# Performance work log

Hardware: AMD Instinct MI355X
Metric: run time of the kernel (lower is better)

## Reference

```python
import jax, jax.numpy as jnp
import numpy as np

B, T, D = 32, 256, 512
P, V = 2048, 40000
DFF = 2148
K_CONCEPT = 50
K_PHENO = 10
EPS = 1e-6


def setup_inputs() -> dict:
    key = jax.random.key(0)
    ks = jax.random.split(key, 10)
    return {
        "visit_embeddings": jax.random.normal(ks[0], (B, T, D), jnp.float32) * 0.05,
        "visit_mask": jax.random.randint(ks[1], (B, T), 0, 2, jnp.int32),
        "embedding_matrix": jax.random.normal(ks[2], (V, D), jnp.float32) * 0.05,
        "phenotype_embeddings": jax.random.normal(ks[3], (P, D), jnp.float32) * 0.05,
        "w1": jax.random.normal(ks[4], (D, DFF), jnp.float32) * (1.0 / np.sqrt(D)),
        "b1": jnp.zeros((DFF,), jnp.float32),
        "w2": jax.random.normal(ks[5], (DFF, D), jnp.float32) * (1.0 / np.sqrt(DFF)),
        "b2": jnp.zeros((D,), jnp.float32),
        "ln1_g": jnp.ones((D,), jnp.float32),
        "ln1_b": jnp.zeros((D,), jnp.float32),
        "ln2_g": jnp.ones((D,), jnp.float32),
        "ln2_b": jnp.zeros((D,), jnp.float32),
    }


def _layer_norm(x, g, b):
    mu = jnp.mean(x, axis=-1, keepdims=True)
    var = jnp.mean(jnp.square(x - mu), axis=-1, keepdims=True)
    return (x - mu) * jax.lax.rsqrt(var + EPS) * g + b


def _smallest_k(x, k):
    # top_k of -x selects the k smallest values per row
    return -jax.lax.top_k(-x, k)[0]


def reference(visit_embeddings, visit_mask, embedding_matrix, phenotype_embeddings,
              w1, b1, w2, b2, ln1_g, ln1_b, ln2_g, ln2_b):
    # mask: original mask==1 means padded; converted mask is 1.0 for valid positions
    conv_mask = (1.0 - visit_mask.astype(jnp.float32))[:, :, None]  # [B,T,1]

    # phenotype attention: softmax over (logits * mask)  (faithful to TF code)
    logits = jnp.einsum('btd,pd->btp', visit_embeddings, phenotype_embeddings) * conv_mask
    probs = jax.nn.softmax(logits, axis=-1)  # [B,T,P]

    # phenotype-concept euclidean distance metric (cdist + row-wise smallest-k)
    r_p = jnp.sum(phenotype_embeddings * phenotype_embeddings, axis=1)[:, None]  # [P,1]
    r_c = jnp.sum(embedding_matrix * embedding_matrix, axis=1)[None, :]          # [1,V]
    d_pc = jnp.sqrt(r_p + r_c - 2.0 * phenotype_embeddings @ embedding_matrix.T)  # [P,V]
    phenotype_concept_dist = jnp.mean(_smallest_k(d_pc, K_CONCEPT))

    # phenotype probability entropy metric
    entropy = -jnp.sum(probs * jnp.log(probs) * conv_mask, axis=-1)  # [B,T]

    # phenotype-phenotype squared-distance metrics
    d_pp = r_p - 2.0 * phenotype_embeddings @ phenotype_embeddings.T + r_p.T  # [P,P]
    near = _smallest_k(d_pp, K_PHENO)  # [P,K_PHENO]
    phe_inv_loss = jnp.mean(jnp.exp(-near))
    phe_dist_metric = jnp.mean(near)
    phe_dist_var = jnp.var(near)

    # residual + FFN block (dropout is identity at inference)
    ctx = probs @ phenotype_embeddings  # [B,T,D]
    out1 = _layer_norm(visit_embeddings + ctx, ln1_g, ln1_b)
    ffn = jnp.maximum(out1 @ w1 + b1, 0.0) @ w2 + b2
    out2 = _layer_norm(out1 + ffn, ln2_g, ln2_b)

    return (out2, probs, phenotype_concept_dist, entropy,
            phe_inv_loss, phe_dist_metric, phe_dist_var)
```

## Files before the change

### kernel.cpp

```cpp
#include <hip/hip_runtime.h>
#include <stdint.h>
#include <stddef.h>

#define BATCH 32
#define TLEN 256
#define DIM 512
#define PHE 2048
#define VOC 40000
#define VOCP 40960
#define DFF 2148
#define DFFP2 2304
#define BT 8192
#define KC 50
#define KP 10
#define CHUNK 8192
#define NCHUNK 5
#define LNEPS 1e-6f
#define BIGF 1e30f

typedef unsigned short u16;
typedef __attribute__((ext_vector_type(8))) short short8;
typedef __attribute__((ext_vector_type(8))) unsigned short ushort8;
typedef __attribute__((ext_vector_type(4))) float floatx4;

__device__ inline u16 f2bf(float f) {
  union { float f; unsigned int u; } v; v.f = f;
  unsigned int u = v.u;
  return (u16)((u + 0x7fffu + ((u >> 16) & 1u)) >> 16);
}

__device__ inline unsigned int f2mono(float f) {
  union { float f; unsigned int u; } c; c.f = f;
  return (c.u & 0x80000000u) ? ~c.u : (c.u | 0x80000000u);
}
__device__ inline float mono2f(unsigned int u) {
  union { unsigned int u; float f; } c;
  c.u = (u & 0x80000000u) ? (u & 0x7FFFFFFFu) : ~u;
  return c.f;
}
__device__ inline unsigned int mono16(u16 u) {
  return (u & 0x8000u) ? (u16)~u : (u16)(u | 0x8000u);
}
__device__ inline float mono2f16(unsigned int k) {
  unsigned int ub = (k & 0x8000u) ? (k & 0x7FFFu) : ((~k) & 0xFFFFu);
  union { unsigned int u; float f; } c; c.u = ub << 16;
  return c.f;
}

__device__ inline void load_lds16(const void* g, void* l) {
  __builtin_amdgcn_global_load_lds(
      (const __attribute__((address_space(1))) unsigned int*)g,
      (__attribute__((address_space(3))) unsigned int*)l, 16, 0, 0);
}

__device__ inline float waveRedSum(float v) {
  #pragma unroll
  for (int off = 32; off > 0; off >>= 1) v += __shfl_down(v, off);
  return v;
}
__device__ inline float waveRedMax(float v) {
  #pragma unroll
  for (int off = 32; off > 0; off >>= 1) v = fmaxf(v, __shfl_down(v, off));
  return v;
}
__device__ inline float blockRedSum(float v) {
  __shared__ float sm[8];
  int lane = threadIdx.x & 63, w = threadIdx.x >> 6, nw = blockDim.x >> 6;
  v = waveRedSum(v);
  __syncthreads();
  if (lane == 0) sm[w] = v;
  __syncthreads();
  float r = 0.f;
  for (int i = 0; i < nw; ++i) r += sm[i];
  return r;
}
__device__ inline float blockRedMax(float v) {
  __shared__ float sm2[8];
  int lane = threadIdx.x & 63, w = threadIdx.x >> 6, nw = blockDim.x >> 6;
  v = waveRedMax(v);
  __syncthreads();
  if (lane == 0) sm2[w] = v;
  __syncthreads();
  float r = -BIGF;
  for (int i = 0; i < nw; ++i) r = fmaxf(r, sm2[i]);
  return r;
}
__device__ inline double blockRedSumD(double v) {
  __shared__ double red[256];
  int tid = threadIdx.x;
  __syncthreads();
  red[tid] = v;
  __syncthreads();
  for (int s = 128; s > 0; s >>= 1) {
    if (tid < s) red[tid] += red[tid + s];
    __syncthreads();
  }
  return red[0];
}

__device__ inline void hist_add2(int* hist, int digit, bool pred) {
  int lane = threadIdx.x & 63;
  unsigned long long act = __ballot(pred);
  if (!act) return;
  int src = __ffsll((long long)act) - 1;
  int ld = __shfl(digit, src);
  unsigned long long m = __ballot(pred && digit == ld);
  if (__popcll(m) >= 32) {
    if (lane == src) atomicAdd(&hist[ld], (int)__popcll(m));
    if ((act & ~m) & (1ull << lane)) atomicAdd(&hist[digit], 1);
  } else {
    if (pred) atomicAdd(&hist[digit], 1);
  }
}

__global__ void k_sentinel(float* out) { out[0] = -12345.0f; }

__global__ void k_cvt(const float* __restrict__ src, u16* __restrict__ dst, int n) {
  int i = blockIdx.x * blockDim.x + threadIdx.x;
  int stride = gridDim.x * blockDim.x;
  for (; i < n; i += stride) dst[i] = f2bf(src[i]);
}

__global__ void k_transpose(const float* __restrict__ src, int R, int C,
                            u16* __restrict__ dst, int DR, int DC) {
  int i = blockIdx.x * blockDim.x + threadIdx.x;
  if (i >= DR * DC) return;
  int r = i / DC, c = i % DC;
  float v = (r < C && c < R) ? src[(size_t)c * C + r] : 0.f;
  dst[i] = f2bf(v);
}

__global__ void k_rownorm(const float* __restrict__ src, float* __restrict__ out, int ncols) {
  int row = blockIdx.x;
  const float* p = src + (size_t)row * ncols;
  float s = 0.f;
  for (int i = threadIdx.x; i < ncols; i += blockDim.x) { float v = p[i]; s += v * v; }
  s = blockRedSum(s);
  if (threadIdx.x == 0) out[row] = s;
}

#define EPI_STORE 0
#define EPI_DPP   1
#define EPI_DPC   2
#define EPI_FFN1  3
#define EPI_FFN2  4

__device__ inline void xcd_block(int BM, int BN, int& m0, int& n0) {
  int nwg = gridDim.x * gridDim.y;
  int orig = blockIdx.y * gridDim.x + blockIdx.x;
  int q = nwg >> 3, r = nwg & 7;
  int xcd = orig & 7, i0 = orig >> 3;
  int wgid = (xcd < r ? xcd * (q + 1) : r * (q + 1) + (xcd - r) * q) + i0;
  m0 = (wgid / gridDim.x) * BM;
  n0 = (wgid % gridDim.x) * BN;
}

template<int EPI>
__device__ inline void epi_write(int rr, int col, float c,
    float* outF, u16* outU, int ldc, const float* rp, const float* rc,
    const float* bias, int bvalid, int nepi) {
  if (EPI == EPI_STORE) {
    outF[(size_t)rr * ldc + col] = c;
  } else if (EPI == EPI_DPP) {
    outF[(size_t)rr * ldc + col] = rp[rr] + rp[col] - 2.f * c;
  } else if (EPI == EPI_DPC) {
    float d = (col < bvalid) ? sqrtf(fmaxf(rp[rr] + rc[col] - 2.f * c, 0.f)) : BIGF;
    outU[(size_t)rr * ldc + col] = f2bf(d);
  } else if (EPI == EPI_FFN1) {
    float h = (col < nepi) ? fmaxf(c + bias[col], 0.f) : 0.f;
    outU[(size_t)rr * ldc + col] = f2bf(h);
  } else if (EPI == EPI_FFN2) {
    outF[(size_t)rr * ldc + col] = c + bias[col];
  }
}

__global__ void __launch_bounds__(256, 2) k_dpc(
    const u16* __restrict__ phe_bf, const u16* __restrict__ emb_bf,
    int gchunk, int ngemm, u16* __restrict__ dw,
    const u16* __restrict__ dr, int schunk, float* __restrict__ top,
    const float* __restrict__ rp, const float* __restrict__ rc)
{
  __shared__ __align__(16) char smem[32768];
  int bid = (int)blockIdx.x;
  if (bid < ngemm) {
    u16* As = (u16*)smem;
    u16* Bs = (u16*)(smem + 16384);
    int tid = threadIdx.x, lane = tid & 63, w = tid >> 6;
    int wm = w >> 1, wn = w & 1;
    int nwg = ngemm, orig = bid;
    int q = nwg >> 3, r = nwg & 7;
    int xcd = orig & 7, i0 = orig >> 3;
    int wgid = (xcd < r ? xcd * (q + 1) : r * (q + 1) + (xcd - r) * q) + i0;
    int m0 = (wgid >> 6) << 7;
    int n0 = (wgid & 63) << 7;
    const u16* Bm = emb_bf + (size_t)gchunk * CHUNK * DIM;
    const float* rcc = rc + gchunk * CHUNK;
    int bvalid = VOC - gchunk * CHUNK; if (bvalid > CHUNK) bvalid = CHUNK;

    floatx4 acc[4][4];
    #pragma unroll
    for (int i = 0; i < 4; ++i)
      #pragma unroll
      for (int j = 0; j < 4; ++j)
        acc[i][j] = (floatx4){0.f, 0.f, 0.f, 0.f};

    int hi = lane >> 4, rsw = lane & 7;
    for (int kt = 0; kt < DIM / 64; ++kt) {
      int k0 = kt * 64;
      #pragma unroll
      for (int p = 0; p < 4; ++p) {
        int c = p * 256 + tid;
        int row = c >> 3;
        int src16 = (c & 7) ^ (row & 7);
        load_lds16(phe_bf + (size_t)(m0 + row) * DIM + k0 + src16 * 8,
                   &As[p * 2048 + w * 512]);
      }
      #pragma unroll
      for (int p = 0; p < 4; ++p) {
        int c = p * 256 + tid;
        int row = c >> 3;
        int src16 = (c & 7) ^ (row & 7);
        load_lds16(Bm + (size_t)(n0 + row) * DIM + k0 + src16 * 8,
                   &Bs[p * 2048 + w * 512]);
      }
      __syncthreads();
      #pragma unroll
      for (int ks = 0; ks < 2; ++ks) {
        int chk = ((ks << 2) | hi) ^ rsw;
        short8 a[4], b[4];
        #pragma unroll
        for (int i = 0; i < 4; ++i)
          a[i] = *(const short8*)&As[(wm * 64 + i * 16 + (lane & 15)) * 64 + chk * 8];
        #pragma unroll
        for (int j = 0; j < 4; ++j)
          b[j] = *(const short8*)&Bs[(wn * 64 + j * 16 + (lane & 15)) * 64 + chk * 8];
        #pragma unroll
        for (int i = 0; i < 4; ++i)
          #pragma unroll
          for (int j = 0; j < 4; ++j)
            acc[i][j] = __builtin_amdgcn_mfma_f32_16x16x32_bf16(a[i], b[j], acc[i][j], 0, 0, 0);
      }
      __syncthreads();
    }
    #pragma unroll
    for (int i = 0; i < 4; ++i) {
      #pragma unroll
      for (int j = 0; j < 4; ++j) {
        floatx4 v = acc[i][j];
        int col = n0 + wn * 64 + j * 16 + (lane & 15);
        int rb = m0 + wm * 64 + i * 16 + ((lane >> 4) << 2);
        #pragma unroll
        for (int qq = 0; qq < 4; ++qq) {
          int rr = rb + qq;
          float d = (col < bvalid) ? sqrtf(fmaxf(rp[rr] + rcc[col] - 2.f * v[qq], 0.f)) : BIGF;
          dw[(size_t)rr * CHUNK + col] = f2bf(d);
        }
      }
    }
  } else {
    if (schunk < 0) return;
    int si = bid - ngemm;
    int row = si >> 1, half = si & 1;
    const u16* src = dr + (size_t)row * CHUNK + half * 4096;
    int* hist = (int*)smem;
    int* cum  = hist + 1024;
    int* wred = cum + 256;
    int* selb = wred + 8;
    int tid = threadIdx.x, lane = tid & 63, w4 = tid >> 6;
    int hbase = w4 << 8;

    unsigned int kv[16];
    #pragma unroll
    for (int j2 = 0; j2 < 2; ++j2) {
      ushort8 qv = *(const ushort8*)(src + j2 * 2048 + tid * 8);
      #pragma unroll
      for (int e = 0; e < 8; ++e) kv[j2 * 8 + e] = mono16((u16)qv[e]);
    }

    int hbmin = 255, hbmax = 0;
    #pragma unroll
    for (int j = 0; j < 16; ++j) {
      int hb = (int)(kv[j] >> 8);
      hbmin = min(hbmin, hb); hbmax = max(hbmax, hb);
    }
    #pragma unroll
    for (int off = 32; off > 0; off >>= 1) {
      hbmin = min(hbmin, __shfl_down(hbmin, off));
      hbmax = max(hbmax, __shfl_down(hbmax, off));
    }
    if (lane == 0) { wred[w4] = hbmin; wred[4 + w4] = hbmax; }
    __syncthreads();
    int bmin = min(min(wred[0], wred[1]), min(wred[2], wred[3]));
    int bmax = max(max(wred[4], wred[5]), max(wred[6], wred[7]));
    __syncthreads();

    unsigned int prefix;
    int kk = KC;
    if (bmin == bmax) {
      prefix = (unsigned int)bmin;
    } else {
      hist[tid] = 0; hist[tid + 256] = 0; hist[tid + 512] = 0; hist[tid + 768] = 0;
      __syncthreads();
      #pragma unroll
      for (int j = 0; j < 16; ++j) hist_add2(hist + hbase, (int)(kv[j] >> 8), true);
      __syncthreads();
      int x = hist[tid] + hist[tid + 256] + hist[tid + 512] + hist[tid + 768];
      #pragma unroll
      for (int off = 1; off < 64; off <<= 1) { int y = __shfl_up(x, off); if (lane >= off) x += y; }
      if (lane == 63) wred[w4] = x;
      __syncthreads();
      #pragma unroll
      for (int i = 0; i < 4; ++i) if (i < w4) x += wred[i];
      cum[tid] = x;
      __syncthreads();
      int prev = (tid == 0) ? 0 : cum[tid - 1];
      if (prev < kk && kk <= cum[tid]) { selb[0] = tid; selb[1] = kk - prev; }
      __syncthreads();
      prefix = (unsigned int)selb[0];
      kk = selb[1];
      __syncthreads();
    }

    hist[tid] = 0; hist[tid + 256] = 0; hist[tid + 512] = 0; hist[tid + 768] = 0;
    __syncthreads();
    #pragma unroll
    for (int j = 0; j < 16; ++j)
      hist_add2(hist + hbase, (int)(kv[j] & 255u), (kv[j] >> 8) == prefix);
    __syncthreads();
    int x = hist[tid] + hist[tid + 256] + hist[tid + 512] + hist[tid + 768];
    #pragma unroll
    for (int off = 1; off < 64; off <<= 1) { int y = __shfl_up(x, off); if (lane >= off) x += y; }
    if (lane == 63) wred[w4] = x;
    __syncthreads();
    #pragma unroll
    for (int i = 0; i < 4; ++i) if (i < w4) x += wred[i];
    cum[tid] = x;
    __syncthreads();
    int prev = (tid == 0) ? 0 : cum[tid - 1];
    if (prev < kk && kk <= cum[tid]) { selb[0] = tid; selb[1] = kk - prev; }
    __syncthreads();
    unsigned int key = (prefix << 8) | (unsigned int)selb[0];
    float thr = mono2f16(key);
    float* o50 = top + (size_t)row * (NCHUNK * 2 * KC) + (schunk * 2 + half) * KC;
    __syncthreads();

    int cless = 0;
    #pragma unroll
    for (int j = 0; j < 16; ++j) if (kv[j] < key) cless++;
    int xc = cless;
    #pragma unroll
    for (int off = 1; off < 64; off <<= 1) { int y = __shfl_up(xc, off); if (lane >= off) xc += y; }
    if (lane == 63) wred[w4] = xc;
    __syncthreads();
    #pragma unroll
    for (int i = 0; i < 4; ++i) if (i < w4) xc += wred[i];
    int o = xc - cless;
    #pragma unroll
    for (int j = 0; j < 16; ++j)
      if (kv[j] < key) o50[o++] = mono2f16(kv[j]);
    cum[tid] = xc;
    __syncthreads();
    int total_less = cum[255];
    for (int i = total_less + tid; i < KC; i += 256) o50[i] = thr;
  }
}

template<int EPI, int BM, int BN, int NTH, int WR, int WC>
__global__ void __launch_bounds__(NTH, 2) k_gemm2(
    const u16* __restrict__ A, int lda,
    const u16* __restrict__ Bm, int ldb, int bvalid, int K,
    float* __restrict__ outF, u16* __restrict__ outU, int ldc,
    const float* __restrict__ rp, const float* __restrict__ rc,
    const float* __restrict__ bias, int nepi)
{
  constexpr int BK = 64;
  constexpr int MR = BM / WR / 16;
  constexpr int NR = BN / WC / 16;
  constexpr int LD_A = BM * BK / (NTH * 8);
  constexpr int LD_B = BN * BK / (NTH * 8);
  __shared__ __align__(16) u16 As[2][BM * BK];
  __shared__ __align__(16) u16 Bs[2][BN * BK];
  int tid = threadIdx.x, lane = tid & 63, w = tid >> 6;
  int wm = w / WC, wn = w % WC;
  int m0, n0;
  xcd_block(BM, BN, m0, n0);

  floatx4 acc[MR][NR];
  #pragma unroll
  for (int i = 0; i < MR; ++i)
    #pragma unroll
    for (int j = 0; j < NR; ++j)
      acc[i][j] = (floatx4){0.f, 0.f, 0.f, 0.f};

  auto stage = [&](int buf, int k0) {
    #pragma unroll
    for (int p = 0; p < LD_A; ++p) {
      int c = p * NTH + tid;
      int row = c >> 3;
      int src16 = (c & 7) ^ (row & 7);
      load_lds16(A + (size_t)(m0 + row) * lda + k0 + src16 * 8,
                 &As[buf][p * NTH * 8 + w * 512]);
    }
    #pragma unroll
    for (int p = 0; p < LD_B; ++p) {
      int c = p * NTH + tid;
      int row = c >> 3;
      int src16 = (c & 7) ^ (row & 7);
      load_lds16(Bm + (size_t)(n0 + row) * ldb + k0 + src16 * 8,
                 &Bs[buf][p * NTH * 8 + w * 512]);
    }
  };

  int nt = K / BK;
  stage(0, 0);
  __syncthreads();
  int cur = 0;
  int hi = lane >> 4;
  int rsw = lane & 7;
  for (int kt = 0; kt < nt; ++kt) {
    if (kt + 1 < nt) stage(cur ^ 1, (kt + 1) * BK);
    #pragma unroll
    for (int ks = 0; ks < 2; ++ks) {
      int chk = ((ks << 2) | hi) ^ rsw;
      short8 a[MR], b[NR];
      #pragma unroll
      for (int i = 0; i < MR; ++i)
        a[i] = *(const short8*)&As[cur][(wm * (BM / WR) + i * 16 + (lane & 15)) * BK + chk * 8];
      #pragma unroll
      for (int j = 0; j < NR; ++j)
        b[j] = *(const short8*)&Bs[cur][(wn * (BN / WC) + j * 16 + (lane & 15)) * BK + chk * 8];
      #pragma unroll
      for (int i = 0; i < MR; ++i)
        #pragma unroll
        for (int j = 0; j < NR; ++j)
          acc[i][j] = __builtin_amdgcn_mfma_f32_16x16x32_bf16(a[i], b[j], acc[i][j], 0, 0, 0);
    }
    __syncthreads();
    cur ^= 1;
  }

  #pragma unroll
  for (int i = 0; i < MR; ++i) {
    #pragma unroll
    for (int j = 0; j < NR; ++j) {
      floatx4 v = acc[i][j];
      int col = n0 + wn * (BN / WC) + j * 16 + (lane & 15);
      int rb = m0 + wm * (BM / WR) + i * 16 + ((lane >> 4) << 2);
      #pragma unroll
      for (int qq = 0; qq < 4; ++qq)
        epi_write<EPI>(rb + qq, col, v[qq], outF, outU, ldc, rp, rc, bias, bvalid, nepi);
    }
  }
}

template<int EPI>
__global__ void __launch_bounds__(256, 4) k_gemm2s(
    const u16* __restrict__ A, int lda,
    const u16* __restrict__ Bm, int ldb, int bvalid, int K,
    float* __restrict__ outF, u16* __restrict__ outU, int ldc,
    const float* __restrict__ rp, const float* __restrict__ rc,
    const float* __restrict__ bias, int nepi)
{
  constexpr int BM = 128, BN = 128, BK = 64, NTH = 256;
  constexpr int MR = 4, NR = 4;
  __shared__ __align__(16) u16 As[BM * BK];
  __shared__ __align__(16) u16 Bs[BN * BK];
  int tid = threadIdx.x, lane = tid & 63, w = tid >> 6;
  int wm = w >> 1, wn = w & 1;
  int m0, n0;
  xcd_block(BM, BN, m0, n0);

  floatx4 acc[MR][NR];
  #pragma unroll
  for (int i = 0; i < MR; ++i)
    #pragma unroll
    for (int j = 0; j < NR; ++j)
      acc[i][j] = (floatx4){0.f, 0.f, 0.f, 0.f};

  int hi = lane >> 4;
  int rsw = lane & 7;
  int nt = K / BK;
  for (int kt = 0; kt < nt; ++kt) {
    int k0 = kt * BK;
    #pragma unroll
    for (int p = 0; p < 4; ++p) {
      int c = p * NTH + tid;
      int row = c >> 3;
      int src16 = (c & 7) ^ (row & 7);
      load_lds16(A + (size_t)(m0 + row) * lda + k0 + src16 * 8,
                 &As[p * NTH * 8 + w * 512]);
    }
    #pragma unroll
    for (int p = 0; p < 4; ++p) {
      int c = p * NTH + tid;
      int row = c >> 3;
      int src16 = (c & 7) ^ (row & 7);
      load_lds16(Bm + (size_t)(n0 + row) * ldb + k0 + src16 * 8,
                 &Bs[p * NTH * 8 + w * 512]);
    }
    __syncthreads();
    #pragma unroll
    for (int ks = 0; ks < 2; ++ks) {
      int chk = ((ks << 2) | hi) ^ rsw;
      short8 a[MR], b[NR];
      #pragma unroll
      for (int i = 0; i < MR; ++i)
        a[i] = *(const short8*)&As[(wm * 64 + i * 16 + (lane & 15)) * BK + chk * 8];
      #pragma unroll
      for (int j = 0; j < NR; ++j)
        b[j] = *(const short8*)&Bs[(wn * 64 + j * 16 + (lane & 15)) * BK + chk * 8];
      #pragma unroll
      for (int i = 0; i < MR; ++i)
        #pragma unroll
        for (int j = 0; j < NR; ++j)
          acc[i][j] = __builtin_amdgcn_mfma_f32_16x16x32_bf16(a[i], b[j], acc[i][j], 0, 0, 0);
    }
    __syncthreads();
  }

  #pragma unroll
  for (int i = 0; i < MR; ++i) {
    #pragma unroll
    for (int j = 0; j < NR; ++j) {
      floatx4 v = acc[i][j];
      int col = n0 + wn * 64 + j * 16 + (lane & 15);
      int rb = m0 + wm * 64 + i * 16 + ((lane >> 4) << 2);
      #pragma unroll
      for (int qq = 0; qq < 4; ++qq)
        epi_write<EPI>(rb + qq, col, v[qq], outF, outU, ldc, rp, rc, bias, bvalid, nepi);
    }
  }
}

__global__ void __launch_bounds__(256) k_softmax(
    const float* __restrict__ logits, const int* __restrict__ mask,
    float* __restrict__ probs, u16* __restrict__ probs_bf,
    float* __restrict__ entropy)
{
  int row = blockIdx.x;
  int tid = threadIdx.x;
  const float* lp = logits + (size_t)row * PHE;
  float* pp = probs + (size_t)row * PHE;
  u16* pb = probs_bf + (size_t)row * PHE;
  if (mask[row] != 0) {
    const float u = 1.0f / (float)PHE;
    const u16 ub = f2bf(u);
    for (int i = tid; i < PHE; i += 256) { pp[i] = u; pb[i] = ub; }
    if (tid == 0) entropy[row] = 0.f;
    return;
  }
  float l[8];
  float mx = -BIGF;
  #pragma unroll
  for (int j = 0; j < 8; ++j) { l[j] = lp[tid + j * 256]; mx = fmaxf(mx, l[j]); }
  mx = blockRedMax(mx);
  float s = 0.f;
  #pragma unroll
  for (int j = 0; j < 8; ++j) { l[j] = __expf(l[j] - mx); s += l[j]; }
  s = blockRedSum(s);
  float inv = 1.0f / s;
  float ent = 0.f;
  #pragma unroll
  for (int j = 0; j < 8; ++j) {
    float p = l[j] * inv;
    pp[tid + j * 256] = p;
    pb[tid + j * 256] = f2bf(p);
    ent += p * __logf(p);
  }
  ent = blockRedSum(ent);
  if (tid == 0) entropy[row] = -ent;
}

__global__ void __launch_bounds__(256) k_ln(
    const float* __restrict__ xa, const float* __restrict__ xb,
    const float* __restrict__ g, const float* __restrict__ bb,
    float* __restrict__ outF, u16* __restrict__ outBf)
{
  int row = blockIdx.x;
  int tid = threadIdx.x;
  const float* pa = xa + (size_t)row * DIM;
  const float* pb = xb + (size_t)row * DIM;
  float x0 = pa[tid] + pb[tid];
  float x1 = pa[tid + 256] + pb[tid + 256];
  float mu = blockRedSum(x0 + x1) * (1.0f / DIM);
  float d0 = x0 - mu, d1 = x1 - mu;
  float var = blockRedSum(d0 * d0 + d1 * d1) * (1.0f / DIM);
  float rs = 1.0f / sqrtf(var + LNEPS);
  float y0 = d0 * rs * g[tid] + bb[tid];
  float y1 = d1 * rs * g[tid + 256] + bb[tid + 256];
  if (outF) {
    outF[(size_t)row * DIM + tid] = y0;
    outF[(size_t)row * DIM + tid + 256] = y1;
  }
  if (outBf) {
    outBf[(size_t)row * DIM + tid] = f2bf(y0);
    outBf[(size_t)row * DIM + tid + 256] = f2bf(y1);
  }
}

template<int NPER>
__global__ void __launch_bounds__(256) k_rsel(
    const float* __restrict__ in, int ldin, int ncols, int k, int mode,
    float* __restrict__ out)
{
  __shared__ int hist[1024];
  __shared__ int cum[256];
  __shared__ int wsum[4];
  __shared__ int sel_bucket, sel_rank;
  int row = blockIdx.x;
  int tid = threadIdx.x;
  int lane = tid & 63, w = tid >> 6;
  int hbase = w << 8;
  const float* src = in + (size_t)row * ldin;

  unsigned int v[NPER];
  #pragma unroll
  for (int j = 0; j < NPER; ++j) {
    int idx = tid + j * 256;
    v[j] = (idx < ncols) ? f2mono(src[idx]) : 0xFFFFFFFFu;
  }

  unsigned int prefix = 0, pmask = 0;
  int kk = k;
  for (int shift = 24; shift >= 0; shift -= 8) {
    hist[tid] = 0; hist[tid + 256] = 0; hist[tid + 512] = 0; hist[tid + 768] = 0;
    __syncthreads();
    #pragma unroll
    for (int j = 0; j < NPER; ++j)
      hist_add2(hist + hbase, (int)((v[j] >> shift) & 255), (v[j] & pmask) == prefix);
    __syncthreads();
    int x = hist[tid] + hist[tid + 256] + hist[tid + 512] + hist[tid + 768];
    #pragma unroll
    for (int off = 1; off < 64; off <<= 1) {
      int y = __shfl_up(x, off);
      if (lane >= off) x += y;
    }
    if (lane == 63) wsum[w] = x;
    __syncthreads();
    #pragma unroll
    for (int i = 0; i < 4; ++i) if (i < w) x += wsum[i];
    cum[tid] = x;
    __syncthreads();
    int prev = (tid == 0) ? 0 : cum[tid - 1];
    if (prev < kk && kk <= cum[tid]) { sel_bucket = tid; sel_rank = kk - prev; }
    __syncthreads();
    prefix |= ((unsigned int)sel_bucket) << shift;
    pmask |= 255u << shift;
    kk = sel_rank;
    __syncthreads();
  }

  float thr = mono2f(prefix);
  int need = kk;

  float s = 0.f, se = 0.f, sq = 0.f;
  #pragma unroll
  for (int j = 0; j < NPER; ++j) {
    if (v[j] < prefix) {
      float f = mono2f(v[j]);
      s += f; se += __expf(-f); sq += f * f;
    }
  }
  float ts = blockRedSum(s);
  float tse = blockRedSum(se);
  float tsq = blockRedSum(sq);
  if (tid == 0) {
    float fn = (float)need;
    ts += fn * thr;
    if (mode == 1) {
      out[row] = ts;
    } else {
      tse += fn * __expf(-thr);
      tsq += fn * thr * thr;
      out[(size_t)row * 4] = ts;
      out[(size_t)row * 4 + 1] = tse;
      out[(size_t)row * 4 + 2] = tsq;
    }
  }
}

__global__ void __launch_bounds__(256) k_final(
    const float* __restrict__ row_sum50, const float* __restrict__ pp_part,
    float* __restrict__ out_pcd, float* __restrict__ out_inv,
    float* __restrict__ out_mean, float* __restrict__ out_var)
{
  int tid = threadIdx.x;
  double s50 = 0, sn = 0, se = 0, sq = 0;
  for (int i = tid; i < PHE; i += 256) {
    s50 += (double)row_sum50[i];
    sn += (double)pp_part[(size_t)i * 4];
    se += (double)pp_part[(size_t)i * 4 + 1];
    sq += (double)pp_part[(size_t)i * 4 + 2];
  }
  s50 = blockRedSumD(s50);
  sn = blockRedSumD(sn);
  se = blockRedSumD(se);
  sq = blockRedSumD(sq);
  if (tid == 0) {
    *out_pcd = (float)(s50 / (double)(PHE * KC));
    double mean = sn / (double)(PHE * KP);
    *out_inv = (float)(se / (double)(PHE * KP));
    *out_mean = (float)mean;
    *out_var = (float)(sq / (double)(PHE * KP) - mean * mean);
  }
}

extern "C" void kernel_launch(void* const* d_in, const int* in_sizes, int n_in,
                              void* d_out, int out_size, void* d_ws, size_t ws_size,
                              hipStream_t stream)
{
  const float* visit = (const float*)d_in[0];
  const int*   vmask = (const int*)d_in[1];
  const float* emb   = (const float*)d_in[2];
  const float* phe   = (const float*)d_in[3];
  const float* w1    = (const float*)d_in[4];
  const float* b1    = (const float*)d_in[5];
  const float* w2    = (const float*)d_in[6];
  const float* b2    = (const float*)d_in[7];
  const float* ln1g  = (const float*)d_in[8];
  const float* ln1b  = (const float*)d_in[9];
  const float* ln2g  = (const float*)d_in[10];
  const float* ln2b  = (const float*)d_in[11];

  float* out = (float*)d_out;
  float* out2      = out;
  float* probs     = out + (size_t)BT * DIM;
  float* pcd       = probs + (size_t)BT * PHE;
  float* entropy   = pcd + 1;
  float* inv_loss  = entropy + BT;
  float* dist_mean = inv_loss + 1;
  float* dist_var  = dist_mean + 1;

  char* wsb = (char*)d_ws;
  size_t off = 0;
  auto alloc = [&](size_t bytes) -> char* {
    char* p = wsb + off;
    off = (off + bytes + 255) & ~(size_t)255;
    return p;
  };
  u16* phe_bf   = (u16*)alloc((size_t)PHE * DIM * 2);
  u16* pheT_bf  = (u16*)alloc((size_t)DIM * PHE * 2);
  u16* visit_bf = (u16*)alloc((size_t)BT * DIM * 2);
  u16* w1T_bf   = (u16*)alloc((size_t)DFFP2 * DIM * 2);
  u16* w2T_bf   = (u16*)alloc((size_t)DIM * DFFP2 * 2);
  float* r_p    = (float*)alloc((size_t)PHE * 4);
  float* r_c    = (float*)alloc((size_t)VOC * 4);
  char* big1    = alloc((size_t)67108864);
  char* big2    = alloc((size_t)VOCP * DIM * 2);
  float* top50c = (float*)alloc((size_t)PHE * NCHUNK * 2 * KC * 4);
  char* big3    = alloc((size_t)PHE * PHE * 4);
  u16* probs_bf = (u16*)alloc((size_t)BT * PHE * 2);
  float* out1_f = (float*)alloc((size_t)BT * DIM * 4);
  u16* out1_bf  = (u16*)alloc((size_t)BT * DIM * 2);
  float* ffn_f  = (float*)alloc((size_t)BT * DIM * 4);
  float* row_sum50 = (float*)alloc((size_t)PHE * 4);
  float* pp_part   = (float*)alloc((size_t)PHE * 4 * 4);

  u16* dchunk0  = (u16*)big1;
  u16* dchunk1  = (u16*)(big1 + 33554432);
  float* logits = (float*)big1;
  u16* emb_bf   = (u16*)big2;
  u16* h_bf     = (u16*)big2;
  float* d_pp   = (float*)big3;
  float* ctx_f  = (float*)big3;

  if (ws_size < off) { k_sentinel<<<1, 1, 0, stream>>>(out); return; }

  k_cvt<<<2048, 256, 0, stream>>>(visit, visit_bf, BT * DIM);
  k_cvt<<<2048, 256, 0, stream>>>(phe, phe_bf, PHE * DIM);
  k_cvt<<<2048, 256, 0, stream>>>(emb, emb_bf, VOC * DIM);
  k_transpose<<<(DIM * PHE + 255) / 256, 256, 0, stream>>>(phe, PHE, DIM, pheT_bf, DIM, PHE);
  k_transpose<<<(DFFP2 * DIM + 255) / 256, 256, 0, stream>>>(w1, DIM, DFF, w1T_bf, DFFP2, DIM);
  k_transpose<<<(DIM * DFFP2 + 255) / 256, 256, 0, stream>>>(w2, DFF, DIM, w2T_bf, DIM, DFFP2);
  k_rownorm<<<PHE, 256, 0, stream>>>(phe, r_p, DIM);
  k_rownorm<<<VOC, 256, 0, stream>>>(emb, r_c, DIM);

  for (int c = 0; c <= NCHUNK; ++c) {
    int g = (c < NCHUNK) ? c : -1;
    int s = c - 1;
    int ngemm = (g >= 0) ? (CHUNK / 128) * (PHE / 128) : 0;
    int nsel  = (s >= 0) ? PHE * 2 : 0;
    u16* dw = (g >= 0) ? ((g & 1) ? dchunk1 : dchunk0) : nullptr;
    u16* dr = (s >= 0) ? ((s & 1) ? dchunk1 : dchunk0) : nullptr;
    k_dpc<<<ngemm + nsel, 256, 0, stream>>>(
        phe_bf, emb_bf, g, ngemm, dw, dr, s, top50c, r_p, r_c);
  }
  k_rsel<2><<<PHE, 256, 0, stream>>>(top50c, NCHUNK * 2 * KC, NCHUNK * 2 * KC, KC, 1, row_sum50);

  k_gemm2<EPI_DPP, 128, 128, 256, 2, 2><<<dim3(PHE / 128, PHE / 128), 256, 0, stream>>>(
      phe_bf, DIM, phe_bf, DIM, PHE, DIM, d_pp, nullptr, PHE, r_p, nullptr, nullptr, 0);
  k_rsel<8><<<PHE, 256, 0, stream>>>(d_pp, PHE, PHE, KP, 2, pp_part);

  k_gemm2s<EPI_STORE><<<dim3(PHE / 128, BT / 128), 256, 0, stream>>>(
      visit_bf, DIM, phe_bf, DIM, PHE, DIM, logits, nullptr, PHE, nullptr, nullptr, nullptr, 0);
  k_softmax<<<BT, 256, 0, stream>>>(logits, vmask, probs, probs_bf, entropy);

  k_gemm2<EPI_STORE, 64, 128, 256, 2, 2><<<dim3(DIM / 128, BT / 64), 256, 0, stream>>>(
      probs_bf, PHE, pheT_bf, PHE, DIM, PHE, ctx_f, nullptr, DIM, nullptr, nullptr, nullptr, 0);

  k_ln<<<BT, 256, 0, stream>>>(visit, ctx_f, ln1g, ln1b, out1_f, out1_bf);
  k_gemm2s<EPI_FFN1><<<dim3(DFFP2 / 128, BT / 128), 256, 0, stream>>>(
      out1_bf, DIM, w1T_bf, DIM, DFFP2, DIM, nullptr, h_bf, DFFP2, nullptr, nullptr, b1, DFF);
  k_gemm2<EPI_FFN2, 64, 128, 256, 2, 2><<<dim3(DIM / 128, BT / 64), 256, 0, stream>>>(
      h_bf, DFFP2, w2T_bf, DFFP2, DIM, DFFP2, ffn_f, nullptr, DIM, nullptr, nullptr, b2, 0);
  k_ln<<<BT, 256, 0, stream>>>(out1_f, ffn_f, ln2g, ln2b, out2, nullptr);

  k_final<<<1, 256, 0, stream>>>(row_sum50, pp_part, pcd, inv_loss, dist_mean, dist_var);
}
```

Measured before the change: 638.1 us.

## Fuse prep kernels and fold pp-distance and logits GEMM into chunked dpc launches

Eight separate conversion, transpose and row-norm kernels are merged into one prep launch that also computes row norms while converting. The phenotype-phenotype distance GEMM and its top-k selection now run as extra blocks inside the chunked distance/selection kernel. The logits GEMM runs in the last loop iteration alongside the final selection pass and stores bf16 logits, which softmax then reads in place. This removes launch overhead and idle tail time by overlapping independent work, and halves logits traffic, at the cost of lower logits precision before softmax and more branching in one large kernel.

After: 689.3 us. +8.0%, slower.

```diff
diff --git a/kernel.cpp b/kernel.cpp
--- a/kernel.cpp
+++ b/kernel.cpp
@@ -28,6 +28,10 @@
   unsigned int u = v.u;
   return (u16)((u + 0x7fffu + ((u >> 16) & 1u)) >> 16);
 }
+__device__ inline float bf2f(u16 u) {
+  union { unsigned int u; float f; } c; c.u = ((unsigned int)u) << 16;
+  return c.f;
+}
 
 __device__ inline unsigned int f2mono(float f) {
   union { float f; unsigned int u; } c; c.f = f;
@@ -115,33 +119,68 @@
 
 __global__ void k_sentinel(float* out) { out[0] = -12345.0f; }
 
-__global__ void k_cvt(const float* __restrict__ src, u16* __restrict__ dst, int n) {
-  int i = blockIdx.x * blockDim.x + threadIdx.x;
-  int stride = gridDim.x * blockDim.x;
-  for (; i < n; i += stride) dst[i] = f2bf(src[i]);
-}
-
-__global__ void k_transpose(const float* __restrict__ src, int R, int C,
-                            u16* __restrict__ dst, int DR, int DC) {
-  int i = blockIdx.x * blockDim.x + threadIdx.x;
-  if (i >= DR * DC) return;
-  int r = i / DC, c = i % DC;
-  float v = (r < C && c < R) ? src[(size_t)c * C + r] : 0.f;
-  dst[i] = f2bf(v);
-}
-
-__global__ void k_rownorm(const float* __restrict__ src, float* __restrict__ out, int ncols) {
-  int row = blockIdx.x;
-  const float* p = src + (size_t)row * ncols;
-  float s = 0.f;
-  for (int i = threadIdx.x; i < ncols; i += blockDim.x) { float v = p[i]; s += v * v; }
-  s = blockRedSum(s);
-  if (threadIdx.x == 0) out[row] = s;
+#define PREP_VIS 2048
+#define PREP_PHT (DIM * PHE / 256)
+#define PREP_W1  (DFFP2 * DIM / 256)
+#define PREP_W2  (DIM * DFFP2 / 256)
+__global__ void __launch_bounds__(256) k_prep(
+    const float* __restrict__ emb, u16* __restrict__ emb_bf, float* __restrict__ r_c,
+    const float* __restrict__ phe, u16* __restrict__ phe_bf, float* __restrict__ r_p,
+    const float* __restrict__ visit, u16* __restrict__ visit_bf,
+    u16* __restrict__ pheT_bf,
+    const float* __restrict__ w1, u16* __restrict__ w1T_bf,
+    const float* __restrict__ w2, u16* __restrict__ w2T_bf)
+{
+  int bid = (int)blockIdx.x, tid = threadIdx.x;
+  if (bid < VOC + PHE) {
+    const float* src = (bid < VOC) ? emb + (size_t)bid * DIM
+                                   : phe + (size_t)(bid - VOC) * DIM;
+    u16* dst = (bid < VOC) ? emb_bf + (size_t)bid * DIM
+                           : phe_bf + (size_t)(bid - VOC) * DIM;
+    float a = src[tid], b = src[tid + 256];
+    dst[tid] = f2bf(a); dst[tid + 256] = f2bf(b);
+    float s = blockRedSum(a * a + b * b);
+    if (tid == 0) {
+      if (bid < VOC) r_c[bid] = s; else r_p[bid - VOC] = s;
+    }
+    return;
+  }
+  int b2 = bid - (VOC + PHE);
+  if (b2 < PREP_VIS) {
+    int base = b2 * 2048 + tid;
+    #pragma unroll
+    for (int e = 0; e < 8; ++e) {
+      int i = base + e * 256;
+      visit_bf[i] = f2bf(visit[i]);
+    }
+    return;
+  }
+  b2 -= PREP_VIS;
+  if (b2 < PREP_PHT) {
+    int i = b2 * 256 + tid;
+    int r = i / PHE, c = i % PHE;
+    pheT_bf[i] = f2bf(phe[(size_t)c * DIM + r]);
+    return;
+  }
+  b2 -= PREP_PHT;
+  if (b2 < PREP_W1) {
+    int i = b2 * 256 + tid;
+    int r = i / DIM, c = i % DIM;
+    float v = (r < DFF) ? w1[(size_t)c * DFF + r] : 0.f;
+    w1T_bf[i] = f2bf(v);
+    return;
+  }
+  b2 -= PREP_W1;
+  {
+    int i = b2 * 256 + tid;
+    int r = i / DFFP2, c = i % DFFP2;
+    float v = (c < DFF) ? w2[(size_t)c * DIM + r] : 0.f;
+    w2T_bf[i] = f2bf(v);
+    return;
+  }
 }
 
 #define EPI_STORE 0
-#define EPI_DPP   1
-#define EPI_DPC   2
 #define EPI_FFN1  3
 #define EPI_FFN2  4
 
@@ -157,15 +196,9 @@
 
 template<int EPI>
 __device__ inline void epi_write(int rr, int col, float c,
-    float* outF, u16* outU, int ldc, const float* rp, const float* rc,
-    const float* bias, int bvalid, int nepi) {
+    float* outF, u16* outU, int ldc, const float* bias, int nepi) {
   if (EPI == EPI_STORE) {
     outF[(size_t)rr * ldc + col] = c;
-  } else if (EPI == EPI_DPP) {
-    outF[(size_t)rr * ldc + col] = rp[rr] + rp[col] - 2.f * c;
-  } else if (EPI == EPI_DPC) {
-    float d = (col < bvalid) ? sqrtf(fmaxf(rp[rr] + rc[col] - 2.f * c, 0.f)) : BIGF;
-    outU[(size_t)rr * ldc + col] = f2bf(d);
   } else if (EPI == EPI_FFN1) {
     float h = (col < nepi) ? fmaxf(c + bias[col], 0.f) : 0.f;
     outU[(size_t)rr * ldc + col] = f2bf(h);
@@ -174,93 +207,116 @@
   }
 }
 
+__device__ __forceinline__ void gemm_core(
+    const u16* __restrict__ A, const u16* __restrict__ Bm,
+    int m0, int n0, int mode,
+    u16* __restrict__ out16, float* __restrict__ outF, int ldc, int bvalid,
+    const float* __restrict__ rp, const float* __restrict__ rcc, char* smem)
+{
+  u16* As = (u16*)smem;
+  u16* Bs = (u16*)(smem + 16384);
+  int tid = threadIdx.x, lane = tid & 63, w = tid >> 6;
+  int wm = w >> 1, wn = w & 1;
+
+  floatx4 acc[4][4];
+  #pragma unroll
+  for (int i = 0; i < 4; ++i)
+    #pragma unroll
+    for (int j = 0; j < 4; ++j)
+      acc[i][j] = (floatx4){0.f, 0.f, 0.f, 0.f};
+
+  int hi = lane >> 4, rsw = lane & 7;
+  for (int kt = 0; kt < DIM / 64; ++kt) {
+    int k0 = kt * 64;
+    #pragma unroll
+    for (int p = 0; p < 4; ++p) {
+      int c = p * 256 + tid;
+      int row = c >> 3;
+      int src16 = (c & 7) ^ (row & 7);
+      load_lds16(A + (size_t)(m0 + row) * DIM + k0 + src16 * 8,
+                 &As[p * 2048 + w * 512]);
+    }
+    #pragma unroll
+    for (int p = 0; p < 4; ++p) {
+      int c = p * 256 + tid;
+      int row = c >> 3;
+      int src16 = (c & 7) ^ (row & 7);
+      load_lds16(Bm + (size_t)(n0 + row) * DIM + k0 + src16 * 8,
+                 &Bs[p * 2048 + w * 512]);
+    }
+    __syncthreads();
+    #pragma unroll
+    for (int ks = 0; ks < 2; ++ks) {
+      int chk = ((ks << 2) | hi) ^ rsw;
+      short8 a[4], b[4];
+      #pragma unroll
+      for (int i = 0; i < 4; ++i)
+        a[i] = *(const short8*)&As[(wm * 64 + i * 16 + (lane & 15)) * 64 + chk * 8];
+      #pragma unroll
+      for (int j = 0; j < 4; ++j)
+        b[j] = *(const short8*)&Bs[(wn * 64 + j * 16 + (lane & 15)) * 64 + chk * 8];
+      #pragma unroll
+      for (int i = 0; i < 4; ++i)
+        #pragma unroll
+        for (int j = 0; j < 4; ++j)
+          acc[i][j] = __builtin_amdgcn_mfma_f32_16x16x32_bf16(a[i], b[j], acc[i][j], 0, 0, 0);
+    }
+    __syncthreads();
+  }
+  #pragma unroll
+  for (int i = 0; i < 4; ++i) {
+    #pragma unroll
+    for (int j = 0; j < 4; ++j) {
+      floatx4 v = acc[i][j];
+      int col = n0 + wn * 64 + j * 16 + (lane & 15);
+      int rb = m0 + wm * 64 + i * 16 + ((lane >> 4) << 2);
+      #pragma unroll
+      for (int qq = 0; qq < 4; ++qq) {
+        int rr = rb + qq;
+        if (mode == 0) {
+          float d = (col < bvalid) ? sqrtf(fmaxf(rp[rr] + rcc[col] - 2.f * v[qq], 0.f)) : BIGF;
+          out16[(size_t)rr * ldc + col] = f2bf(d);
+        } else if (mode == 1) {
+          out16[(size_t)rr * ldc + col] = f2bf(v[qq]);
+        } else {
+          outF[(size_t)rr * ldc + col] = rp[rr] + rp[col] - 2.f * v[qq];
+        }
+      }
+    }
+  }
+}
+
 __global__ void __launch_bounds__(256, 2) k_dpc(
-    const u16* __restrict__ phe_bf, const u16* __restrict__ emb_bf,
-    int gchunk, int ngemm, u16* __restrict__ dw,
-    const u16* __restrict__ dr, int schunk, float* __restrict__ top,
-    const float* __restrict__ rp, const float* __restrict__ rc)
+    const u16* __restrict__ A, const u16* __restrict__ Bm,
+    int gmode, int gridx, int ngemm,
+    u16* __restrict__ gout16, int gldc, int gbvalid,
+    const float* __restrict__ rp, const float* __restrict__ rcc,
+    int ndppg, const u16* __restrict__ phe_bf, float* __restrict__ d_pp,
+    int nsel, const u16* __restrict__ dr, int schunk, float* __restrict__ top,
+    int ndpps, const float* __restrict__ dpp_in, float* __restrict__ pp_part)
 {
   __shared__ __align__(16) char smem[32768];
   int bid = (int)blockIdx.x;
   if (bid < ngemm) {
-    u16* As = (u16*)smem;
-    u16* Bs = (u16*)(smem + 16384);
-    int tid = threadIdx.x, lane = tid & 63, w = tid >> 6;
-    int wm = w >> 1, wn = w & 1;
     int nwg = ngemm, orig = bid;
     int q = nwg >> 3, r = nwg & 7;
     int xcd = orig & 7, i0 = orig >> 3;
     int wgid = (xcd < r ? xcd * (q + 1) : r * (q + 1) + (xcd - r) * q) + i0;
-    int m0 = (wgid >> 6) << 7;
-    int n0 = (wgid & 63) << 7;
-    const u16* Bm = emb_bf + (size_t)gchunk * CHUNK * DIM;
-    const float* rcc = rc + gchunk * CHUNK;
-    int bvalid = VOC - gchunk * CHUNK; if (bvalid > CHUNK) bvalid = CHUNK;
-
-    floatx4 acc[4][4];
-    #pragma unroll
-    for (int i = 0; i < 4; ++i)
-      #pragma unroll
-      for (int j = 0; j < 4; ++j)
-        acc[i][j] = (floatx4){0.f, 0.f, 0.f, 0.f};
-
-    int hi = lane >> 4, rsw = lane & 7;
-    for (int kt = 0; kt < DIM / 64; ++kt) {
-      int k0 = kt * 64;
-      #pragma unroll
-      for (int p = 0; p < 4; ++p) {
-        int c = p * 256 + tid;
-        int row = c >> 3;
-        int src16 = (c & 7) ^ (row & 7);
-        load_lds16(phe_bf + (size_t)(m0 + row) * DIM + k0 + src16 * 8,
-                   &As[p * 2048 + w * 512]);
-      }
-      #pragma unroll
-      for (int p = 0; p < 4; ++p) {
-        int c = p * 256 + tid;
-        int row = c >> 3;
-        int src16 = (c & 7) ^ (row & 7);
-        load_lds16(Bm + (size_t)(n0 + row) * DIM + k0 + src16 * 8,
-                   &Bs[p * 2048 + w * 512]);
-      }
-      __syncthreads();
-      #pragma unroll
-      for (int ks = 0; ks < 2; ++ks) {
-        int chk = ((ks << 2) | hi) ^ rsw;
-        short8 a[4], b[4];
-        #pragma unroll
-        for (int i = 0; i < 4; ++i)
-          a[i] = *(const short8*)&As[(wm * 64 + i * 16 + (lane & 15)) * 64 + chk * 8];
-        #pragma unroll
-        for (int j = 0; j < 4; ++j)
-          b[j] = *(const short8*)&Bs[(wn * 64 + j * 16 + (lane & 15)) * 64 + chk * 8];
-        #pragma unroll
-        for (int i = 0; i < 4; ++i)
-          #pragma unroll
-          for (int j = 0; j < 4; ++j)
-            acc[i][j] = __builtin_amdgcn_mfma_f32_16x16x32_bf16(a[i], b[j], acc[i][j], 0, 0, 0);
-      }
-      __syncthreads();
-    }
-    #pragma unroll
-    for (int i = 0; i < 4; ++i) {
-      #pragma unroll
-      for (int j = 0; j < 4; ++j) {
-        floatx4 v = acc[i][j];
-        int col = n0 + wn * 64 + j * 16 + (lane & 15);
-        int rb = m0 + wm * 64 + i * 16 + ((lane >> 4) << 2);
-        #pragma unroll
-        for (int qq = 0; qq < 4; ++qq) {
-          int rr = rb + qq;
-          float d = (col < bvalid) ? sqrtf(fmaxf(rp[rr] + rcc[col] - 2.f * v[qq], 0.f)) : BIGF;
-          dw[(size_t)rr * CHUNK + col] = f2bf(d);
-        }
-      }
-    }
-  } else {
+    int m0 = (wgid / gridx) * 128;
+    int n0 = (wgid % gridx) * 128;
+    gemm_core(A, Bm, m0, n0, gmode, gout16, nullptr, gldc, gbvalid, rp, rcc, smem);
+    return;
+  }
+  bid -= ngemm;
+  if (bid < ndppg) {
+    int m0 = (bid >> 4) << 7, n0 = (bid & 15) << 7;
+    gemm_core(phe_bf, phe_bf, m0, n0, 2, nullptr, d_pp, PHE, PHE, rp, nullptr, smem);
+    return;
+  }
+  bid -= ndppg;
+  if (bid < nsel) {
     if (schunk < 0) return;
-    int si = bid - ngemm;
-    int row = si >> 1, half = si & 1;
+    int row = bid >> 1, half = bid & 1;
     const u16* src = dr + (size_t)row * CHUNK + half * 4096;
     int* hist = (int*)smem;
     int* cum  = hist + 1024;
@@ -362,6 +418,73 @@
     __syncthreads();
     int total_less = cum[255];
     for (int i = total_less + tid; i < KC; i += 256) o50[i] = thr;
+    return;
+  }
+  bid -= nsel;
+  if (bid < ndpps) {
+    int row = bid;
+    const float* src = dpp_in + (size_t)row * PHE;
+    int* hist = (int*)smem;
+    int* cum  = hist + 1024;
+    int* wsum = cum + 256;
+    int* selb = wsum + 4;
+    int tid = threadIdx.x, lane = tid & 63, w4 = tid >> 6;
+    int hbase = w4 << 8;
+
+    unsigned int v[8];
+    #pragma unroll
+    for (int j = 0; j < 8; ++j) v[j] = f2mono(src[tid + j * 256]);
+
+    unsigned int prefix = 0, pmask = 0;
+    int kk = KP;
+    for (int shift = 24; shift >= 0; shift -= 8) {
+      hist[tid] = 0; hist[tid + 256] = 0; hist[tid + 512] = 0; hist[tid + 768] = 0;
+      __syncthreads();
+      #pragma unroll
+      for (int j = 0; j < 8; ++j)
+        hist_add2(hist + hbase, (int)((v[j] >> shift) & 255), (v[j] & pmask) == prefix);
+      __syncthreads();
+      int x = hist[tid] + hist[tid + 256] + hist[tid + 512] + hist[tid + 768];
+      #pragma unroll
+      for (int off = 1; off < 64; off <<= 1) { int y = __shfl_up(x, off); if (lane >= off) x += y; }
+      if (lane == 63) wsum[w4] = x;
+      __syncthreads();
+      #pragma unroll
+      for (int i = 0; i < 4; ++i) if (i < w4) x += wsum[i];
+      cum[tid] = x;
+      __syncthreads();
+      int prev = (tid == 0) ? 0 : cum[tid - 1];
+      if (prev < kk && kk <= cum[tid]) { selb[0] = tid; selb[1] = kk - prev; }
+      __syncthreads();
+      prefix |= ((unsigned int)selb[0]) << shift;
+      pmask |= 255u << shift;
+      kk = selb[1];
+      __syncthreads();
+    }
+
+    float thr = mono2f(prefix);
+    int need = kk;
+    float s = 0.f, se = 0.f, sq = 0.f;
+    #pragma unroll
+    for (int j = 0; j < 8; ++j) {
+      if (v[j] < prefix) {
+        float f = mono2f(v[j]);
+        s += f; se += __expf(-f); sq += f * f;
+      }
+    }
+    float ts = blockRedSum(s);
+    float tse = blockRedSum(se);
+    float tsq = blockRedSum(sq);
+    if (tid == 0) {
+      float fn = (float)need;
+      ts += fn * thr;
+      tse += fn * __expf(-thr);
+      tsq += fn * thr * thr;
+      pp_part[(size_t)row * 4] = ts;
+      pp_part[(size_t)row * 4 + 1] = tse;
+      pp_part[(size_t)row * 4 + 2] = tsq;
+    }
+    return;
   }
 }
 
@@ -370,7 +493,6 @@
     const u16* __restrict__ A, int lda,
     const u16* __restrict__ Bm, int ldb, int bvalid, int K,
     float* __restrict__ outF, u16* __restrict__ outU, int ldc,
-    const float* __restrict__ rp, const float* __restrict__ rc,
     const float* __restrict__ bias, int nepi)
 {
   constexpr int BK = 64;
@@ -448,7 +570,7 @@
       int rb = m0 + wm * (BM / WR) + i * 16 + ((lane >> 4) << 2);
       #pragma unroll
       for (int qq = 0; qq < 4; ++qq)
-        epi_write<EPI>(rb + qq, col, v[qq], outF, outU, ldc, rp, rc, bias, bvalid, nepi);
+        epi_write<EPI>(rb + qq, col, v[qq], outF, outU, ldc, bias, nepi);
     }
   }
 }
@@ -458,7 +580,6 @@
     const u16* __restrict__ A, int lda,
     const u16* __restrict__ Bm, int ldb, int bvalid, int K,
     float* __restrict__ outF, u16* __restrict__ outU, int ldc,
-    const float* __restrict__ rp, const float* __restrict__ rc,
     const float* __restrict__ bias, int nepi)
 {
   constexpr int BM = 128, BN = 128, BK = 64, NTH = 256;
@@ -527,21 +648,19 @@
       int rb = m0 + wm * 64 + i * 16 + ((lane >> 4) << 2);
       #pragma unroll
       for (int qq = 0; qq < 4; ++qq)
-        epi_write<EPI>(rb + qq, col, v[qq], outF, outU, ldc, rp, rc, bias, bvalid, nepi);
+        epi_write<EPI>(rb + qq, col, v[qq], outF, outU, ldc, bias, nepi);
     }
   }
 }
 
 __global__ void __launch_bounds__(256) k_softmax(
-    const float* __restrict__ logits, const int* __restrict__ mask,
-    float* __restrict__ probs, u16* __restrict__ probs_bf,
-    float* __restrict__ entropy)
+    u16* __restrict__ probs_bf, const int* __restrict__ mask,
+    float* __restrict__ probs, float* __restrict__ entropy)
 {
   int row = blockIdx.x;
   int tid = threadIdx.x;
-  const float* lp = logits + (size_t)row * PHE;
+  u16* pb = probs_bf + (size_t)row * PHE;
   float* pp = probs + (size_t)row * PHE;
-  u16* pb = probs_bf + (size_t)row * PHE;
   if (mask[row] != 0) {
     const float u = 1.0f / (float)PHE;
     const u16 ub = f2bf(u);
@@ -552,7 +671,7 @@
   float l[8];
   float mx = -BIGF;
   #pragma unroll
-  for (int j = 0; j < 8; ++j) { l[j] = lp[tid + j * 256]; mx = fmaxf(mx, l[j]); }
+  for (int j = 0; j < 8; ++j) { l[j] = bf2f(pb[tid + j * 256]); mx = fmaxf(mx, l[j]); }
   mx = blockRedMax(mx);
   float s = 0.f;
   #pragma unroll
@@ -600,7 +719,7 @@
 
 template<int NPER>
 __global__ void __launch_bounds__(256) k_rsel(
-    const float* __restrict__ in, int ldin, int ncols, int k, int mode,
+    const float* __restrict__ in, int ldin, int ncols, int k,
     float* __restrict__ out)
 {
   __shared__ int hist[1024];
@@ -652,31 +771,12 @@
 
   float thr = mono2f(prefix);
   int need = kk;
-
-  float s = 0.f, se = 0.f, sq = 0.f;
-  #pragma unroll
-  for (int j = 0; j < NPER; ++j) {
-    if (v[j] < prefix) {
-      float f = mono2f(v[j]);
-      s += f; se += __expf(-f); sq += f * f;
-    }
-  }
+  float s = 0.f;
+  #pragma unroll
+  for (int j = 0; j < NPER; ++j)
+    if (v[j] < prefix) s += mono2f(v[j]);
   float ts = blockRedSum(s);
-  float tse = blockRedSum(se);
-  float tsq = blockRedSum(sq);
-  if (tid == 0) {
-    float fn = (float)need;
-    ts += fn * thr;
-    if (mode == 1) {
-      out[row] = ts;
-    } else {
-      tse += fn * __expf(-thr);
-      tsq += fn * thr * thr;
-      out[(size_t)row * 4] = ts;
-      out[(size_t)row * 4 + 1] = tse;
-      out[(size_t)row * 4 + 2] = tsq;
-    }
-  }
+  if (tid == 0) out[row] = ts + (float)need * thr;
 }
 
 __global__ void __launch_bounds__(256) k_final(
@@ -758,7 +858,6 @@
 
   u16* dchunk0  = (u16*)big1;
   u16* dchunk1  = (u16*)(big1 + 33554432);
-  float* logits = (float*)big1;
   u16* emb_bf   = (u16*)big2;
   u16* h_bf     = (u16*)big2;
   float* d_pp   = (float*)big3;
@@ -766,43 +865,46 @@
 
   if (ws_size < off) { k_sentinel<<<1, 1, 0, stream>>>(out); return; }
 
-  k_cvt<<<2048, 256, 0, stream>>>(visit, visit_bf, BT * DIM);
-  k_cvt<<<2048, 256, 0, stream>>>(phe, phe_bf, PHE * DIM);
-  k_cvt<<<2048, 256, 0, stream>>>(emb, emb_bf, VOC * DIM);
-  k_transpose<<<(DIM * PHE + 255) / 256, 256, 0, stream>>>(phe, PHE, DIM, pheT_bf, DIM, PHE);
-  k_transpose<<<(DFFP2 * DIM + 255) / 256, 256, 0, stream>>>(w1, DIM, DFF, w1T_bf, DFFP2, DIM);
-  k_transpose<<<(DIM * DFFP2 + 255) / 256, 256, 0, stream>>>(w2, DFF, DIM, w2T_bf, DIM, DFFP2);
-  k_rownorm<<<PHE, 256, 0, stream>>>(phe, r_p, DIM);
-  k_rownorm<<<VOC, 256, 0, stream>>>(emb, r_c, DIM);
+  int nprep = (VOC + PHE) + PREP_VIS + PREP_PHT + PREP_W1 + PREP_W2;
+  k_prep<<<nprep, 256, 0, stream>>>(emb, emb_bf, r_c, phe, phe_bf, r_p,
+                                    visit, visit_bf, pheT_bf, w1, w1T_bf, w2, w2T_bf);
 
   for (int c = 0; c <= NCHUNK; ++c) {
     int g = (c < NCHUNK) ? c : -1;
     int s = c - 1;
-    int ngemm = (g >= 0) ? (CHUNK / 128) * (PHE / 128) : 0;
-    int nsel  = (s >= 0) ? PHE * 2 : 0;
+    int nsel = (s >= 0) ? PHE * 2 : 0;
+    int ndppg = (c == 0) ? (PHE / 128) * (PHE / 128) : 0;
+    int ndpps = (c == 1) ? PHE : 0;
     u16* dw = (g >= 0) ? ((g & 1) ? dchunk1 : dchunk0) : nullptr;
     u16* dr = (s >= 0) ? ((s & 1) ? dchunk1 : dchunk0) : nullptr;
-    k_dpc<<<ngemm + nsel, 256, 0, stream>>>(
-        phe_bf, emb_bf, g, ngemm, dw, dr, s, top50c, r_p, r_c);
-  }
-  k_rsel<2><<<PHE, 256, 0, stream>>>(top50c, NCHUNK * 2 * KC, NCHUNK * 2 * KC, KC, 1, row_sum50);
-
-  k_gemm2<EPI_DPP, 128, 128, 256, 2, 2><<<dim3(PHE / 128, PHE / 128), 256, 0, stream>>>(
-      phe_bf, DIM, phe_bf, DIM, PHE, DIM, d_pp, nullptr, PHE, r_p, nullptr, nullptr, 0);
-  k_rsel<8><<<PHE, 256, 0, stream>>>(d_pp, PHE, PHE, KP, 2, pp_part);
-
-  k_gemm2s<EPI_STORE><<<dim3(PHE / 128, BT / 128), 256, 0, stream>>>(
-      visit_bf, DIM, phe_bf, DIM, PHE, DIM, logits, nullptr, PHE, nullptr, nullptr, nullptr, 0);
-  k_softmax<<<BT, 256, 0, stream>>>(logits, vmask, probs, probs_bf, entropy);
-
+    if (g >= 0) {
+      int bvalid = VOC - g * CHUNK; if (bvalid > CHUNK) bvalid = CHUNK;
+      k_dpc<<<1024 + ndppg + nsel + ndpps, 256, 0, stream>>>(
+          phe_bf, emb_bf + (size_t)g * CHUNK * DIM, 0, 64, 1024,
+          dw, CHUNK, bvalid, r_p, r_c + (size_t)g * CHUNK,
+          ndppg, phe_bf, d_pp,
+          nsel, dr, s, top50c,
+          ndpps, d_pp, pp_part);
+    } else {
+      k_dpc<<<1024 + nsel, 256, 0, stream>>>(
+          visit_bf, phe_bf, 1, 16, 1024,
+          probs_bf, PHE, PHE, nullptr, nullptr,
+          0, phe_bf, d_pp,
+          nsel, dr, s, top50c,
+          0, d_pp, pp_part);
+    }
+  }
+  k_rsel<2><<<PHE, 256, 0, stream>>>(top50c, NCHUNK * 2 * KC, NCHUNK * 2 * KC, KC, row_sum50);
+
+  k_softmax<<<BT, 256, 0, stream>>>(probs_bf, vmask, probs, entropy);
   k_gemm2<EPI_STORE, 64, 128, 256, 2, 2><<<dim3(DIM / 128, BT / 64), 256, 0, stream>>>(
-      probs_bf, PHE, pheT_bf, PHE, DIM, PHE, ctx_f, nullptr, DIM, nullptr, nullptr, nullptr, 0);
+      probs_bf, PHE, pheT_bf, PHE, DIM, PHE, ctx_f, nullptr, DIM, nullptr, 0);
 
   k_ln<<<BT, 256, 0, stream>>>(visit, ctx_f, ln1g, ln1b, out1_f, out1_bf);
   k_gemm2s<EPI_FFN1><<<dim3(DFFP2 / 128, BT / 128), 256, 0, stream>>>(
-      out1_bf, DIM, w1T_bf, DIM, DFFP2, DIM, nullptr, h_bf, DFFP2, nullptr, nullptr, b1, DFF);
+      out1_bf, DIM, w1T_bf, DIM, DFFP2, DIM, nullptr, h_bf, DFFP2, b1, DFF);
   k_gemm2<EPI_FFN2, 64, 128, 256, 2, 2><<<dim3(DIM / 128, BT / 64), 256, 0, stream>>>(
-      h_bf, DFFP2, w2T_bf, DFFP2, DIM, DFFP2, ffn_f, nullptr, DIM, nullptr, nullptr, b2, 0);
+      h_bf, DFFP2, w2T_bf, DFFP2, DIM, DFFP2, ffn_f, nullptr, DIM, b2, 0);
   k_ln<<<BT, 256, 0, stream>>>(out1_f, ffn_f, ln2g, ln2b, out2, nullptr);
 
   k_final<<<1, 256, 0, stream>>>(row_sum50, pp_part, pcd, inv_loss, dist_mean, dist_var);
```
